# Kernel tuning notes

Hardware: AMD Instinct MI355X
Metric: run time of the kernel (lower is better)

Reference implementation:

```python
import jax, jax.numpy as jnp
import numpy as np

# Geometry / model constants
WD, WH, WW = 2, 7, 7          # window size
SD, SH, SW = 1, 3, 3          # shift size
DIM, NH = 96, 3               # channels per half, heads
HD = DIM // NH                # head dim = 32
MLP = 4 * DIM
B, D, H, W = 2, 16, 56, 56    # D,H,W divisible by window -> no padding
N = WD * WH * WW              # tokens per window = 98
NWIN = (D // WD) * (H // WH) * (W // WW)  # 512


def window_partition(x):
    # x: [b, d, h, w, c] -> [b*nW, N, c]  (works for np and jnp arrays)
    b, d, h, w, c = x.shape
    x = x.reshape(b, d // WD, WD, h // WH, WH, w // WW, WW, c)
    return x.transpose(0, 1, 3, 5, 2, 4, 6, 7).reshape(-1, N, c)


def window_reverse(win, b, d, h, w):
    # [b*nW, N, c] -> [b, d, h, w, c]
    c = win.shape[-1]
    x = win.reshape(b, d // WD, h // WH, w // WW, WD, WH, WW, c)
    return x.transpose(0, 1, 4, 2, 5, 3, 6, 7).reshape(b, d, h, w, c)


def _rel_index():
    coords = np.stack(np.meshgrid(np.arange(WD), np.arange(WH), np.arange(WW), indexing='ij'))
    coords = coords.reshape(3, -1)                      # [3, N]
    rel = (coords[:, :, None] - coords[:, None, :]).transpose(1, 2, 0)  # [N, N, 3]
    rel[:, :, 0] += WD - 1; rel[:, :, 1] += WH - 1; rel[:, :, 2] += WW - 1
    rel[:, :, 0] *= (2 * WH - 1) * (2 * WW - 1)
    rel[:, :, 1] *= (2 * WW - 1)
    return rel.sum(-1).astype(np.int32)                 # [N, N]


def _compute_mask():
    img = np.zeros((1, D, H, W, 1), np.float32)
    cnt = 0
    for d in (slice(0, -WD), slice(-WD, -SD), slice(-SD, None)):
        for h in (slice(0, -WH), slice(-WH, -SH), slice(-SH, None)):
            for w in (slice(0, -WW), slice(-WW, -SW), slice(-SW, None)):
                img[:, d, h, w, :] = cnt; cnt += 1
    mw = window_partition(img).squeeze(-1)              # [nW, N]
    diff = mw[:, None, :] - mw[:, :, None]
    return np.where(diff != 0, np.float32(-100.0), np.float32(0.0))


def layernorm(x, g, b, eps=1e-5):
    m = x.mean(-1, keepdims=True)
    v = ((x - m) ** 2).mean(-1, keepdims=True)
    return (x - m) * jax.lax.rsqrt(v + eps) * g + b


def setup_inputs() -> dict:
    key = jax.random.key(0)
    ks = jax.random.split(key, 8)
    s = 0.02
    return {
        'x': jax.random.normal(ks[0], (B, D, H, W, 2 * DIM), jnp.float32),
        'mask_matrix': jnp.asarray(_compute_mask()),
        'rel_index': jnp.asarray(_rel_index()),
        'norm1_g': jnp.ones((DIM,), jnp.float32), 'norm1_b': jnp.zeros((DIM,), jnp.float32),
        'qkv_w': s * jax.random.normal(ks[1], (3 * DIM, DIM), jnp.float32),
        'qkv_b': jnp.zeros((3 * DIM,), jnp.float32),
        'rel_bias_table': s * jax.random.normal(ks[2], ((2 * WD - 1) * (2 * WH - 1) * (2 * WW - 1), NH), jnp.float32),
        'proj_w': s * jax.random.normal(ks[3], (DIM, DIM), jnp.float32),
        'proj_b': jnp.zeros((DIM,), jnp.float32),
        'norm2_g': jnp.ones((DIM,), jnp.float32), 'norm2_b': jnp.zeros((DIM,), jnp.float32),
        'fc1_w': s * jax.random.normal(ks[4], (MLP, DIM), jnp.float32),
        'fc1_b': jnp.zeros((MLP,), jnp.float32),
        'fc2_w': s * jax.random.normal(ks[5], (DIM, MLP), jnp.float32),
        'fc2_b': jnp.zeros((DIM,), jnp.float32),
    }


def reference(x, mask_matrix, rel_index, norm1_g, norm1_b, qkv_w, qkv_b,
              rel_bias_table, proj_w, proj_b, norm2_g, norm2_b,
              fc1_w, fc1_b, fc2_w, fc2_b):
    x1, x2 = jnp.split(x, 2, axis=-1)                   # each [B,D,H,W,DIM]

    # ---- F branch: shifted windowed attention on x2 ----
    xn = layernorm(x2, norm1_g, norm1_b)
    shifted = jnp.roll(xn, (-SD, -SH, -SW), axis=(1, 2, 3))
    xw = window_partition(shifted)                      # [B*nW, N, DIM]
    qkv = (xw @ qkv_w.T + qkv_b).reshape(-1, N, 3, NH, HD).transpose(2, 0, 3, 1, 4)
    q, k, v = qkv[0], qkv[1], qkv[2]                    # [B*nW, NH, N, HD]
    attn = jnp.einsum('bhnd,bhmd->bhnm', q, k) * (HD ** -0.5)
    bias = rel_bias_table[rel_index.reshape(-1)].reshape(N, N, NH).transpose(2, 0, 1)
    attn = attn + bias[None]
    attn = attn.reshape(B, NWIN, NH, N, N) + mask_matrix[None, :, None]
    attn = jax.nn.softmax(attn.reshape(-1, NH, N, N), axis=-1)
    out = jnp.einsum('bhnm,bhmd->bhnd', attn, v).transpose(0, 2, 1, 3).reshape(-1, N, DIM)
    out = out @ proj_w.T + proj_b
    out = window_reverse(out, B, D, H, W)
    out = jnp.roll(out, (SD, SH, SW), axis=(1, 2, 3))
    y1 = x1 + out

    # ---- G branch: MLP on y1 ----
    g = layernorm(y1, norm2_g, norm2_b)
    g = jax.nn.gelu(g @ fc1_w.T + fc1_b, approximate=False) @ fc2_w.T + fc2_b
    y2 = x2 + g

    return jnp.concatenate([y1, y2], axis=-1)
```

## Files before the change

### kernel.cpp

```cpp
#include <hip/hip_runtime.h>
#include <math.h>

typedef unsigned int u32;
typedef unsigned short u16;

typedef __attribute__((ext_vector_type(8))) short bf16x8;
typedef __attribute__((ext_vector_type(4))) float f32x4;

#define NTOK 98
#define NWIN 1024

#define XS_STR 104
#define QK_STR 40
#define P_STR  136
#define Q_BASE 13328
#define K_BASE 17808
#define VT_BASE 22288
#define LDS_U16 26640

#define COMB_U16 344064

__device__ __forceinline__ float bflo(u32 u){ union{u32 i; float f;} c; c.i = u<<16; return c.f; }
__device__ __forceinline__ float bfhi(u32 u){ union{u32 i; float f;} c; c.i = u & 0xffff0000u; return c.f; }
__device__ __forceinline__ u16 f2bf(float f){
  union{float f; u32 i;} c; c.f = f;
  u32 x = c.i;
  return (u16)((x + 0x7fffu + ((x>>16)&1u)) >> 16);
}

__device__ __forceinline__ float gelu_f(float v){
  float t = __expf(-1.702f * v);
  return v * __builtin_amdgcn_rcpf(1.f + t);
}

__device__ __forceinline__ int src_token(int win, int t){
  int b  = win >> 9;
  int wr = win & 511;
  int db = wr >> 6, hb = (wr >> 3) & 7, wb = wr & 7;
  int di = t / 49, r = t - di*49;
  int hi = r / 7,  wi = r - hi*7;
  int d = (db*2 + di + 1) & 15;
  int h = hb*7 + hi + 3; if (h >= 56) h -= 56;
  int w = wb*7 + wi + 3; if (w >= 56) w -= 56;
  return ((b*16 + d)*56 + h)*56 + w;
}

__global__ __launch_bounds__(256) void k0_prep(const float* __restrict__ qkvw,
    const float* __restrict__ qkvb, const float* __restrict__ pw,
    const float* __restrict__ w1, const float* __restrict__ w2,
    u16* __restrict__ Wb, float* __restrict__ bs){
  int i = blockIdx.x*256 + threadIdx.x;
  if (i < 288*96){
    float v = qkvw[i];
    if (i < 96*96) v *= 0.17677669529663687f;
    Wb[i] = f2bf(v);
  } else if (i < 288*96 + 96*96){
    Wb[i] = f2bf(pw[i - 288*96]);
  } else if (i < 288*96 + 96*96 + 384*96){
    Wb[i] = f2bf(w1[i - (288*96 + 96*96)]);
  } else if (i < 288*96 + 96*96 + 384*96 + 96*384){
    Wb[i] = f2bf(w2[i - (288*96 + 96*96 + 384*96)]);
  }
  if (i < 288){
    float v = qkvb[i];
    if (i < 96) v *= 0.17677669529663687f;
    bs[i] = v;
  }
}

__global__ __launch_bounds__(256) void k0b_comb(const float* __restrict__ bias_tab,
    const int* __restrict__ rel_idx, const float* __restrict__ mask,
    u16* __restrict__ comb){
  int idx = blockIdx.x*256 + threadIdx.x;
  if (idx >= COMB_U16) return;
  int m   = idx / 43008;  int r1 = idx - m*43008;
  int hd  = r1 / 14336;   int r2 = r1 - hd*14336;
  int mt  = r2 / 2048;    int r3 = r2 - mt*2048;
  int rr  = r3 / 512;     int r4 = r3 - rr*512;
  int ntp = r4 / 128;     int r5 = r4 - ntp*128;
  int ln  = r5 >> 1;      int half = r5 & 1;
  int lg  = ln >> 4,      l15 = ln & 15;
  int nt  = ntp*2 + half;
  int i   = mt*16 + lg*4 + rr;
  int j   = nt*16 + l15;
  float v = -1e30f;
  if (i < 98 && j < 98){
    int wr = ((m>>2)&1)*448 + ((m>>1)&1)*56 + (m&1)*7;
    v = bias_tab[rel_idx[i*98+j]*3 + hd] + mask[(size_t)wr*9604 + i*98 + j];
  }
  comb[idx] = f2bf(v);
}

__global__ __launch_bounds__(256) void k1_ln(const float* __restrict__ x,
      const float* __restrict__ g, const float* __restrict__ bb, u16* __restrict__ xn){
  int wid  = (blockIdx.x << 2) + (threadIdx.x >> 6);
  int lane = threadIdx.x & 63;
  if (wid >= NWIN*NTOK) return;
  int win = wid / NTOK, t = wid - win*NTOK;
  int tok = src_token(win, t);
  const float* xp = x + (size_t)tok*192 + 96;
  float a0 = 0.f, a1 = 0.f;
  if (lane < 48){ float2 v = *(const float2*)(xp + (lane<<1)); a0 = v.x; a1 = v.y; }
  float s = a0 + a1, s2 = a0*a0 + a1*a1;
  #pragma unroll
  for (int o = 32; o; o >>= 1){ s += __shfl_xor(s, o); s2 += __shfl_xor(s2, o); }
  float mean = s * (1.f/96.f);
  float rstd = rsqrtf(s2*(1.f/96.f) - mean*mean + 1e-5f);
  if (lane < 48){
    float r0 = (a0-mean)*rstd*g[2*lane]   + bb[2*lane];
    float r1 = (a1-mean)*rstd*g[2*lane+1] + bb[2*lane+1];
    u32 pk = (u32)f2bf(r0) | ((u32)f2bf(r1) << 16);
    *(u32*)(xn + (size_t)wid*96 + (lane<<1)) = pk;
  }
}

__global__ __launch_bounds__(256) void k2_attn(const u16* __restrict__ xn,
    const u16* __restrict__ Wb, const float* __restrict__ bs,
    const u16* __restrict__ comb, u16* __restrict__ attn_o){
  __shared__ __align__(16) u16 lds[LDS_U16];
  int tid  = threadIdx.x;
  int lane = tid & 63, wv = tid >> 6;
  int l15  = lane & 15, lg = lane >> 4;
  int j = blockIdx.x;
  int group = j / 24, r24 = j - group*24;
  int win = group*8 + (r24 & 7);
  int hd  = r24 >> 3;

  {
    const u32* xw = (const u32*)(xn + (size_t)win*98*96);
    u32* xs32 = (u32*)lds;
    for (int i = tid; i < 98*48; i += 256){
      int r = i/48, c = i - r*48;
      xs32[r*52 + c] = xw[i];
    }
    for (int i = tid; i < 14*52; i += 256){
      int r = 98 + i/52, c = i - (i/52)*52;
      xs32[r*52 + c] = 0;
    }
    u32* vt32 = (u32*)(lds + VT_BASE);
    for (int i = tid; i < 32*12; i += 256){
      int d = i/12, c = i - d*12;
      vt32[d*68 + 56 + c] = 0;
    }
  }
  __syncthreads();

  for (int t = wv; t < 42; t += 4){
    f32x4 acc = {0.f,0.f,0.f,0.f};
    if (t < 28){
      int tt = (t < 14) ? t : t - 14;
      int mt = tt >> 1, nt = tt & 1;
      int ch = hd*32 + nt*16 + l15 + ((t < 14) ? 0 : 96);
      const u16* wrow = Wb + ch*96 + lg*8;
      const u16* xsrow = lds + (mt*16 + l15)*XS_STR;
      #pragma unroll
      for (int ks = 0; ks < 3; ks++){
        bf16x8 a = *(const bf16x8*)(xsrow + ks*32 + lg*8);
        bf16x8 b = *(const bf16x8*)(wrow + ks*32);
        acc = __builtin_amdgcn_mfma_f32_16x16x32_bf16(a, b, acc, 0, 0, 0);
      }
      float bias = bs[ch];
      u16* dst = lds + ((t < 14) ? Q_BASE : K_BASE);
      int col = nt*16 + l15;
      int rbase = mt*16 + lg*4;
      #pragma unroll
      for (int r = 0; r < 4; r++)
        dst[(rbase+r)*QK_STR + col] = f2bf(acc[r] + bias);
    } else {
      int tt = t - 28; int mt = tt/7, nt = tt - mt*7;
      int ch = 192 + hd*32 + mt*16 + l15;
      const u16* wrow = Wb + ch*96 + lg*8;
      const u16* xsrow = lds + (nt*16 + l15)*XS_STR;
      #pragma unroll
      for (int ks = 0; ks < 3; ks++){
        bf16x8 a = *(const bf16x8*)(wrow + ks*32);
        bf16x8 b = *(const bf16x8*)(xsrow + ks*32 + lg*8);
        acc = __builtin_amdgcn_mfma_f32_16x16x32_bf16(a, b, acc, 0, 0, 0);
      }
      int dbase = mt*16 + lg*4;
      #pragma unroll
      for (int r = 0; r < 4; r++){
        float bias = bs[192 + hd*32 + dbase + r];
        lds[VT_BASE + (dbase+r)*P_STR + nt*16 + l15] = f2bf(acc[r] + bias);
      }
    }
  }
  __syncthreads();

  {
    int wr = win & 511;
    int maskid = ((wr>>6)==7)*4 + (((wr>>3)&7)==7)*2 + ((wr&7)==7);
    const u32* cb_base = (const u32*)comb + (size_t)(maskid*3 + hd)*7168 + lane;

    for (int mt = wv; mt < 7; mt += 4){
      {
        u32* p32 = (u32*)lds;
        int rmax = (mt == 6) ? 2 : 16;
        for (int i = lane; i < rmax*12; i += 64){
          int rr = i/12, c = i - rr*12;
          p32[(mt*16+rr)*68 + 56 + c] = 0;
        }
      }
      int ibase = mt*16 + lg*4;
      const u32* cbm = cb_base + mt*1024;
      float cb[4][7];
      #pragma unroll
      for (int r = 0; r < 4; r++){
        #pragma unroll
        for (int ntp = 0; ntp < 4; ntp++){
          u32 pk = cbm[(r*4 + ntp)*64];
          cb[r][2*ntp] = bflo(pk);
          if (2*ntp + 1 < 7) cb[r][2*ntp+1] = bfhi(pk);
        }
      }
      const u16* qrow = lds + Q_BASE + (mt*16 + l15)*QK_STR;
      bf16x8 a = *(const bf16x8*)(qrow + lg*8);
      f32x4 s[7];
      #pragma unroll
      for (int nt = 0; nt < 7; nt++){
        const u16* krow = lds + K_BASE + (nt*16 + l15)*QK_STR;
        bf16x8 b = *(const bf16x8*)(krow + lg*8);
        f32x4 z = {0.f,0.f,0.f,0.f};
        s[nt] = __builtin_amdgcn_mfma_f32_16x16x32_bf16(a, b, z, 0, 0, 0);
      }
      #pragma unroll
      for (int r = 0; r < 4; r++){
        int i = ibase + r;
        float sv[7];
        float mx = -3.0e38f;
        #pragma unroll
        for (int nt = 0; nt < 7; nt++){
          float v = s[nt][r] + cb[r][nt];
          sv[nt] = v; mx = fmaxf(mx, v);
        }
        #pragma unroll
        for (int off = 1; off < 16; off <<= 1) mx = fmaxf(mx, __shfl_xor(mx, off));
        float sum = 0.f;
        #pragma unroll
        for (int nt = 0; nt < 7; nt++){
          float e = __expf(sv[nt] - mx);
          sv[nt] = e; sum += e;
        }
        #pragma unroll
        for (int off = 1; off < 16; off <<= 1) sum += __shfl_xor(sum, off);
        float inv = 1.f / sum;
        if (i < 98){
          #pragma unroll
          for (int nt = 0; nt < 7; nt++)
            lds[i*P_STR + nt*16 + l15] = f2bf(sv[nt]*inv);
        }
      }
    }
  }
  __syncthreads();

  for (int t = wv; t < 14; t += 4){
    int mt = t >> 1, nt = t & 1;
    const u16* prow = lds + (mt*16 + l15)*P_STR;
    const u16* vrow = lds + VT_BASE + (nt*16 + l15)*P_STR;
    f32x4 acc = {0.f,0.f,0.f,0.f};
    #pragma unroll
    for (int ks = 0; ks < 4; ks++){
      bf16x8 a = *(const bf16x8*)(prow + ks*32 + lg*8);
      bf16x8 b = *(const bf16x8*)(vrow + ks*32 + lg*8);
      acc = __builtin_amdgcn_mfma_f32_16x16x32_bf16(a, b, acc, 0, 0, 0);
    }
    int ibase = mt*16 + lg*4;
    int d = nt*16 + l15;
    #pragma unroll
    for (int r = 0; r < 4; r++){
      int i = ibase + r;
      if (i < 98) attn_o[((size_t)win*98 + i)*96 + hd*32 + d] = f2bf(acc[r]);
    }
  }
}

#define HS 392
#define X1F_U16 3328
#define YN_U16 12544
#define S_U16 12544
#define WT_U16 18816
__global__ __launch_bounds__(256, 4) void k34_projmlp(const u16* __restrict__ attn_o,
    const u16* __restrict__ Pwb, const float* __restrict__ pb,
    const float* __restrict__ g2, const float* __restrict__ b2,
    const u16* __restrict__ W1b, const float* __restrict__ b1,
    const u16* __restrict__ W2b, const float* __restrict__ bb2,
    const float* __restrict__ x, float* __restrict__ out){
  __shared__ __align__(16) u16 lds[18880];
  int tid = threadIdx.x;
  int lane = tid & 63, wv = tid >> 6;
  int l15 = lane & 15, lg = lane >> 4;
  size_t base = (size_t)blockIdx.x * 32;
  float* x1f = (float*)(lds + X1F_U16);
  float* resf = (float*)lds;
  u16* S = lds + S_U16;
  int* wt_s = (int*)(lds + WT_U16);
  int mt = wv & 1, kh = wv >> 1;

  if (tid < 32){
    int tok = (int)base + tid;
    int b = tok / 50176; int r0 = tok - b*50176;
    int d = r0 / 3136;   int r1 = r0 - d*3136;
    int h = r1 / 56;     int w = r1 - h*56;
    int dd = (d + 15) & 15;
    int db = dd >> 1, di = dd & 1;
    int hh = h - 3; if (hh < 0) hh += 56;
    int hb = hh / 7, hi = hh - hb*7;
    int ww = w - 3; if (ww < 0) ww += 56;
    int wb = ww / 7, wi = ww - wb*7;
    wt_s[tid] = (b*512 + db*64 + hb*8 + wb)*98 + di*49 + hi*7 + wi;
  }
  __syncthreads();

  {
    const u32* src = (const u32*)attn_o;
    u32* aw32 = (u32*)lds;
    #pragma unroll
    for (int k = 0; k < 6; k++){
      int i = tid + k*256;
      int r = i/48, c = i - r*48;
      aw32[r*52 + c] = src[(size_t)wt_s[r]*48 + c];
    }
    #pragma unroll
    for (int k = 0; k < 3; k++){
      int i = tid + k*256;
      int tk = i/24, c4 = i - tk*24;
      float4 v = *(const float4*)(x + (base + tk)*192 + c4*4);
      *(float4*)(x1f + tk*100 + c4*4) = v;
    }
  }
  __syncthreads();

  {
    const u16* a0p = lds + l15*104 + lg*8;
    const u16* a1p = a0p + 16*104;
    bf16x8 a00=*(const bf16x8*)(a0p), a01=*(const bf16x8*)(a0p+32), a02=*(const bf16x8*)(a0p+64);
    bf16x8 a10=*(const bf16x8*)(a1p), a11=*(const bf16x8*)(a1p+32), a12=*(const bf16x8*)(a1p+64);
    for (int nt = wv; nt < 6; nt += 4){
      const u16* wrow = Pwb + (nt*16 + l15)*96 + lg*8;
      bf16x8 w0=*(const bf16x8*)(wrow), w1=*(const bf16x8*)(wrow+32), w2=*(const bf16x8*)(wrow+64);
      f32x4 acc0 = {0.f,0.f,0.f,0.f}, acc1 = {0.f,0.f,0.f,0.f};
      acc0 = __builtin_amdgcn_mfma_f32_16x16x32_bf16(a00, w0, acc0, 0, 0, 0);
      acc1 = __builtin_amdgcn_mfma_f32_16x16x32_bf16(a10, w0, acc1, 0, 0, 0);
      acc0 = __builtin_amdgcn_mfma_f32_16x16x32_bf16(a01, w1, acc0, 0, 0, 0);
      acc1 = __builtin_amdgcn_mfma_f32_16x16x32_bf16(a11, w1, acc1, 0, 0, 0);
      acc0 = __builtin_amdgcn_mfma_f32_16x16x32_bf16(a02, w2, acc0, 0, 0, 0);
      acc1 = __builtin_amdgcn_mfma_f32_16x16x32_bf16(a12, w2, acc1, 0, 0, 0);
      int n = nt*16 + l15;
      float bias = pb[n];
      #pragma unroll
      for (int r = 0; r < 4; r++){
        int row = lg*4 + r;
        x1f[row*100 + n] = acc0[r] + bias + x1f[row*100 + n];
      }
      #pragma unroll
      for (int r = 0; r < 4; r++){
        int row = 16 + lg*4 + r;
        x1f[row*100 + n] = acc1[r] + bias + x1f[row*100 + n];
      }
    }
  }
  __syncthreads();

  {
    #pragma unroll
    for (int k = 0; k < 3; k++){
      int i = tid + k*256;
      int tk = i/24, c4 = i - tk*24;
      *(float4*)(out + (base + tk)*192 + c4*4) = *(const float4*)(x1f + tk*100 + c4*4);
    }
    int tk = tid >> 3, c8 = tid & 7;
    const float4* yp = (const float4*)(x1f + tk*100 + c8*12);
    float4 v4[3];
    #pragma unroll
    for (int j = 0; j < 3; j++) v4[j] = yp[j];
    float s = 0.f, s2 = 0.f;
    #pragma unroll
    for (int j = 0; j < 3; j++){
      s  += v4[j].x + v4[j].y + v4[j].z + v4[j].w;
      s2 += v4[j].x*v4[j].x + v4[j].y*v4[j].y + v4[j].z*v4[j].z + v4[j].w*v4[j].w;
    }
    s  += __shfl_xor(s, 1);  s  += __shfl_xor(s, 2);  s  += __shfl_xor(s, 4);
    s2 += __shfl_xor(s2, 1); s2 += __shfl_xor(s2, 2); s2 += __shfl_xor(s2, 4);
    float mean = s * (1.f/96.f);
    float rstd = rsqrtf(s2*(1.f/96.f) - mean*mean + 1e-5f);
    u32* dst = (u32*)(lds + YN_U16) + tk*52 + c8*6;
    const float* gp = g2 + c8*12;
    const float* bp = b2 + c8*12;
    #pragma unroll
    for (int p = 0; p < 6; p++){
      float e0 = (p & 1) ? v4[p>>1].z : v4[p>>1].x;
      float e1 = (p & 1) ? v4[p>>1].w : v4[p>>1].y;
      float r0 = (e0 - mean)*rstd*gp[2*p]   + bp[2*p];
      float r1 = (e1 - mean)*rstd*gp[2*p+1] + bp[2*p+1];
      dst[p] = (u32)f2bf(r0) | ((u32)f2bf(r1) << 16);
    }
  }
  __syncthreads();

  bf16x8 a00, a01, a02, a10, a11, a12;
  {
    const u16* a0p = lds + YN_U16 + l15*104 + lg*8;
    const u16* a1p = a0p + 16*104;
    a00 = *(const bf16x8*)(a0p); a01 = *(const bf16x8*)(a0p+32); a02 = *(const bf16x8*)(a0p+64);
    a10 = *(const bf16x8*)(a1p); a11 = *(const bf16x8*)(a1p+32); a12 = *(const bf16x8*)(a1p+64);
  }
  __syncthreads();

  for (int c = 0; c < 6; c++){
    {
      const u32* srcw = (const u32*)(W1b + c*64*96);
      u32* dstw = (u32*)S;
      #pragma unroll
      for (int k = 0; k < 12; k++) dstw[tid + k*256] = srcw[tid + k*256];
    }
    __syncthreads();
    {
      const u16* wrow = S + (wv*16 + l15)*96 + lg*8;
      bf16x8 w0=*(const bf16x8*)(wrow), w1=*(const bf16x8*)(wrow+32), w2=*(const bf16x8*)(wrow+64);
      f32x4 acc0 = {0.f,0.f,0.f,0.f}, acc1 = {0.f,0.f,0.f,0.f};
      acc0 = __builtin_amdgcn_mfma_f32_16x16x32_bf16(a00, w0, acc0, 0, 0, 0);
      acc1 = __builtin_amdgcn_mfma_f32_16x16x32_bf16(a10, w0, acc1, 0, 0, 0);
      acc0 = __builtin_amdgcn_mfma_f32_16x16x32_bf16(a01, w1, acc0, 0, 0, 0);
      acc1 = __builtin_amdgcn_mfma_f32_16x16x32_bf16(a11, w1, acc1, 0, 0, 0);
      acc0 = __builtin_amdgcn_mfma_f32_16x16x32_bf16(a02, w2, acc0, 0, 0, 0);
      acc1 = __builtin_amdgcn_mfma_f32_16x16x32_bf16(a12, w2, acc1, 0, 0, 0);
      int n = (c*4 + wv)*16 + l15;
      float bias = b1[n];
      #pragma unroll
      for (int r = 0; r < 4; r++)
        lds[(lg*4 + r)*HS + n] = f2bf(gelu_f(acc0[r] + bias));
      #pragma unroll
      for (int r = 0; r < 4; r++)
        lds[(16 + lg*4 + r)*HS + n] = f2bf(gelu_f(acc1[r] + bias));
    }
    __syncthreads();
  }

  f32x4 res0, res1, res2, res3, res4, res5;
  #pragma unroll
  for (int c = 0; c < 6; c++){
    {
      const u32* srcw = (const u32*)(W2b + c*16*384);
      u32* dstw = (u32*)S;
      #pragma unroll
      for (int k = 0; k < 12; k++){
        int i = tid + k*256;
        int row = i / 192, col = i - row*192;
        dstw[row*196 + col] = srcw[i];
      }
    }
    __syncthreads();
    {
      const u16* arow = lds + (mt*16 + l15)*HS + kh*192 + lg*8;
      const u16* wrow = S + l15*392 + kh*192 + lg*8;
      f32x4 acc = {0.f,0.f,0.f,0.f};
      #pragma unroll
      for (int ks = 0; ks < 6; ks++){
        bf16x8 xa = *(const bf16x8*)(arow + ks*32);
        bf16x8 wa = *(const bf16x8*)(wrow + ks*32);
        acc = __builtin_amdgcn_mfma_f32_16x16x32_bf16(xa, wa, acc, 0, 0, 0);
      }
      if (c == 0) res0 = acc; else if (c == 1) res1 = acc;
      else if (c == 2) res2 = acc; else if (c == 3) res3 = acc;
      else if (c == 4) res4 = acc; else res5 = acc;
    }
    __syncthreads();
  }

  if (kh == 0){
    #pragma unroll
    for (int c = 0; c < 6; c++){
      f32x4 rc = (c==0)?res0:(c==1)?res1:(c==2)?res2:(c==3)?res3:(c==4)?res4:res5;
      int col = c*16 + l15;
      float bias = bb2[col];
      #pragma unroll
      for (int r = 0; r < 4; r++)
        resf[(mt*16 + lg*4 + r)*100 + col] = rc[r] + bias;
    }
  }
  __syncthreads();
  if (kh == 1){
    #pragma unroll
    for (int c = 0; c < 6; c++){
      f32x4 rc = (c==0)?res0:(c==1)?res1:(c==2)?res2:(c==3)?res3:(c==4)?res4:res5;
      int col = c*16 + l15;
      #pragma unroll
      for (int r = 0; r < 4; r++)
        resf[(mt*16 + lg*4 + r)*100 + col] += rc[r];
    }
  }
  __syncthreads();

  {
    #pragma unroll
    for (int k = 0; k < 3; k++){
      int i = tid + k*256;
      int tk = i/24, c4 = i - tk*24;
      float4 a = *(const float4*)(resf + tk*100 + c4*4);
      float4 b = *(const float4*)(x + (base + tk)*192 + 96 + c4*4);
      float4 o; o.x = a.x + b.x; o.y = a.y + b.y; o.z = a.z + b.z; o.w = a.w + b.w;
      *(float4*)(out + (base + tk)*192 + 96 + c4*4) = o;
    }
  }
}

extern "C" void kernel_launch(void* const* d_in, const int* in_sizes, int n_in,
                              void* d_out, int out_size, void* d_ws, size_t ws_size,
                              hipStream_t stream){
  const float* x    = (const float*)d_in[0];
  const float* mask = (const float*)d_in[1];
  const int*   reli = (const int*)d_in[2];
  const float* n1g  = (const float*)d_in[3];
  const float* n1b  = (const float*)d_in[4];
  const float* qkvw = (const float*)d_in[5];
  const float* qkvb = (const float*)d_in[6];
  const float* btab = (const float*)d_in[7];
  const float* pw   = (const float*)d_in[8];
  const float* pb   = (const float*)d_in[9];
  const float* n2g  = (const float*)d_in[10];
  const float* n2b  = (const float*)d_in[11];
  const float* w1   = (const float*)d_in[12];
  const float* b1   = (const float*)d_in[13];
  const float* w2   = (const float*)d_in[14];
  const float* b2   = (const float*)d_in[15];
  float* out = (float*)d_out;

  u16* xn   = (u16*)d_ws;
  u16* attn = xn + (size_t)NWIN*98*96;
  u16* Wb   = attn + (size_t)NWIN*98*96;
  u16* Pwb  = Wb + 288*96;
  u16* W1b  = Pwb + 96*96;
  u16* W2b  = W1b + 384*96;
  float* bsc = (float*)(W2b + 96*384);
  u16* comb = (u16*)(bsc + 288);

  k0_prep<<<432,   256, 0, stream>>>(qkvw, qkvb, pw, w1, w2, Wb, bsc);
  k0b_comb<<<1344, 256, 0, stream>>>(btab, reli, mask, comb);
  k1_ln  <<<25088, 256, 0, stream>>>(x, n1g, n1b, xn);
  k2_attn<<<3072,  256, 0, stream>>>(xn, Wb, bsc, comb, attn);
  k34_projmlp<<<3136, 256, 0, stream>>>(attn, Pwb, pb, n2g, n2b,
                                        W1b, b1, W2b, b2, x, out);
}
```

Baseline: 161.7 us.

## Register-prefetch MLP weight chunks and pad W1 LDS rows in projmlp kernel

```diff
diff --git a/kernel.cpp b/kernel.cpp
--- a/kernel.cpp
+++ b/kernel.cpp
@@ -279,14 +279,14 @@
 #define X1F_U16 3328
 #define YN_U16 12544
 #define S_U16 12544
-#define WT_U16 18816
+#define WT_U16 19200
 __global__ __launch_bounds__(256, 4) void k34_projmlp(const u16* __restrict__ attn_o,
     const u16* __restrict__ Pwb, const float* __restrict__ pb,
     const float* __restrict__ g2, const float* __restrict__ b2,
     const u16* __restrict__ W1b, const float* __restrict__ b1,
     const u16* __restrict__ W2b, const float* __restrict__ bb2,
     const float* __restrict__ x, float* __restrict__ out){
-  __shared__ __align__(16) u16 lds[18880];
+  __shared__ __align__(16) u16 lds[19264];
   int tid = threadIdx.x;
   int lane = tid & 63, wv = tid >> 6;
   int l15 = lane & 15, lg = lane >> 4;
@@ -294,6 +294,7 @@
   float* x1f = (float*)(lds + X1F_U16);
   float* resf = (float*)lds;
   u16* S = lds + S_U16;
+  u32* S32 = (u32*)S;
   int* wt_s = (int*)(lds + WT_U16);
   int mt = wv & 1, kh = wv >> 1;
 
@@ -405,18 +406,26 @@
     a00 = *(const bf16x8*)(a0p); a01 = *(const bf16x8*)(a0p+32); a02 = *(const bf16x8*)(a0p+64);
     a10 = *(const bf16x8*)(a1p); a11 = *(const bf16x8*)(a1p+32); a12 = *(const bf16x8*)(a1p+64);
   }
-  __syncthreads();
-
-  for (int c = 0; c < 6; c++){
+  const u32* w1src = (const u32*)W1b;
+  u32 pA[12], pB[12];
+  #pragma unroll
+  for (int k = 0; k < 12; k++) pA[k] = w1src[tid + k*256];
+  __syncthreads();
+
+  #pragma unroll
+  for (int cc = 0; cc < 3; cc++){
+    int c = cc*2;
+    #pragma unroll
+    for (int k = 0; k < 12; k++){
+      int i = tid + k*256;
+      int row = i/48, col = i - row*48;
+      S32[row*52 + col] = pA[k];
+    }
+    #pragma unroll
+    for (int k = 0; k < 12; k++) pB[k] = w1src[(c+1)*3072 + tid + k*256];
+    __syncthreads();
     {
-      const u32* srcw = (const u32*)(W1b + c*64*96);
-      u32* dstw = (u32*)S;
-      #pragma unroll
-      for (int k = 0; k < 12; k++) dstw[tid + k*256] = srcw[tid + k*256];
-    }
-    __syncthreads();
-    {
-      const u16* wrow = S + (wv*16 + l15)*96 + lg*8;
+      const u16* wrow = S + (wv*16 + l15)*104 + lg*8;
       bf16x8 w0=*(const bf16x8*)(wrow), w1=*(const bf16x8*)(wrow+32), w2=*(const bf16x8*)(wrow+64);
       f32x4 acc0 = {0.f,0.f,0.f,0.f}, acc1 = {0.f,0.f,0.f,0.f};
       acc0 = __builtin_amdgcn_mfma_f32_16x16x32_bf16(a00, w0, acc0, 0, 0, 0);
@@ -435,21 +444,55 @@
         lds[(16 + lg*4 + r)*HS + n] = f2bf(gelu_f(acc1[r] + bias));
     }
     __syncthreads();
-  }
-
+    #pragma unroll
+    for (int k = 0; k < 12; k++){
+      int i = tid + k*256;
+      int row = i/48, col = i - row*48;
+      S32[row*52 + col] = pB[k];
+    }
+    if (cc < 2){
+      #pragma unroll
+      for (int k = 0; k < 12; k++) pA[k] = w1src[(c+2)*3072 + tid + k*256];
+    } else {
+      #pragma unroll
+      for (int k = 0; k < 12; k++) pA[k] = ((const u32*)W2b)[tid + k*256];
+    }
+    __syncthreads();
+    {
+      const u16* wrow = S + (wv*16 + l15)*104 + lg*8;
+      bf16x8 w0=*(const bf16x8*)(wrow), w1=*(const bf16x8*)(wrow+32), w2=*(const bf16x8*)(wrow+64);
+      f32x4 acc0 = {0.f,0.f,0.f,0.f}, acc1 = {0.f,0.f,0.f,0.f};
+      acc0 = __builtin_amdgcn_mfma_f32_16x16x32_bf16(a00, w0, acc0, 0, 0, 0);
+      acc1 = __builtin_amdgcn_mfma_f32_16x16x32_bf16(a10, w0, acc1, 0, 0, 0);
+      acc0 = __builtin_amdgcn_mfma_f32_16x16x32_bf16(a01, w1, acc0, 0, 0, 0);
+      acc1 = __builtin_amdgcn_mfma_f32_16x16x32_bf16(a11, w1, acc1, 0, 0, 0);
+      acc0 = __builtin_amdgcn_mfma_f32_16x16x32_bf16(a02, w2, acc0, 0, 0, 0);
+      acc1 = __builtin_amdgcn_mfma_f32_16x16x32_bf16(a12, w2, acc1, 0, 0, 0);
+      int n = ((c+1)*4 + wv)*16 + l15;
+      float bias = b1[n];
+      #pragma unroll
+      for (int r = 0; r < 4; r++)
+        lds[(lg*4 + r)*HS + n] = f2bf(gelu_f(acc0[r] + bias));
+      #pragma unroll
+      for (int r = 0; r < 4; r++)
+        lds[(16 + lg*4 + r)*HS + n] = f2bf(gelu_f(acc1[r] + bias));
+    }
+    __syncthreads();
+  }
+
+  const u32* w2src = (const u32*)W2b;
   f32x4 res0, res1, res2, res3, res4, res5;
   #pragma unroll
-  for (int c = 0; c < 6; c++){
-    {
-      const u32* srcw = (const u32*)(W2b + c*16*384);
-      u32* dstw = (u32*)S;
-      #pragma unroll
-      for (int k = 0; k < 12; k++){
-        int i = tid + k*256;
-        int row = i / 192, col = i - row*192;
-        dstw[row*196 + col] = srcw[i];
-      }
-    }
+  for (int cc = 0; cc < 3; cc++){
+    int c = cc*2;
+    #pragma unroll
+    for (int k = 0; k < 12; k++){
+      int i = tid + k*256;
+      int row = i/192, col = i - row*192;
+      S32[row*196 + col] = pA[k];
+    }
+    #pragma unroll
+    for (int k = 0; k < 12; k++) pB[k] = w2src[(c+1)*3072 + tid + k*256];
     __syncthreads();
     {
       const u16* arow = lds + (mt*16 + l15)*HS + kh*192 + lg*8;
@@ -461,9 +504,31 @@
         bf16x8 wa = *(const bf16x8*)(wrow + ks*32);
         acc = __builtin_amdgcn_mfma_f32_16x16x32_bf16(xa, wa, acc, 0, 0, 0);
       }
-      if (c == 0) res0 = acc; else if (c == 1) res1 = acc;
-      else if (c == 2) res2 = acc; else if (c == 3) res3 = acc;
-      else if (c == 4) res4 = acc; else res5 = acc;
+      if (cc == 0) res0 = acc; else if (cc == 1) res2 = acc; else res4 = acc;
+    }
+    __syncthreads();
+    #pragma unroll
+    for (int k = 0; k < 12; k++){
+      int i = tid + k*256;
+      int row = i/192, col = i - row*192;
+      S32[row*196 + col] = pB[k];
+    }
+    if (cc < 2){
+      #pragma unroll
+      for (int k = 0; k < 12; k++) pA[k] = w2src[(c+2)*3072 + tid + k*256];
+    }
+    __syncthreads();
+    {
+      const u16* arow = lds + (mt*16 + l15)*HS + kh*192 + lg*8;
+      const u16* wrow = S + l15*392 + kh*192 + lg*8;
+      f32x4 acc = {0.f,0.f,0.f,0.f};
+      #pragma unroll
+      for (int ks = 0; ks < 6; ks++){
+        bf16x8 xa = *(const bf16x8*)(arow + ks*32);
+        bf16x8 wa = *(const bf16x8*)(wrow + ks*32);
+        acc = __builtin_amdgcn_mfma_f32_16x16x32_bf16(xa, wa, acc, 0, 0, 0);
+      }
+      if (cc == 0) res1 = acc; else if (cc == 1) res3 = acc; else res5 = acc;
     }
     __syncthreads();
   }
```

Result: no change. 162.4 us (+0.4%).
